# Kernel optimization log

Hardware: AMD Instinct MI355X
Metric: run time of the kernel (lower is better)

## Reference

```python
import jax, jax.numpy as jnp
import numpy as np

EPS = 1e-05  # matches module EPS buffer

def setup_inputs() -> dict:
    key = jax.random.key(0)
    ks = jax.random.split(key, 7)
    B, IN, OUT = 1024, 4096, 4096
    init_log_std = np.log(0.0005).astype(np.float32)
    return {
        "x": jax.random.normal(ks[0], (B, IN), dtype=jnp.float32),
        "weight_mean": jax.random.normal(ks[1], (OUT, IN), dtype=jnp.float32) * (IN ** -0.5),
        "weight_std_param": jnp.full((OUT, IN), init_log_std, dtype=jnp.float32) + 0.01 * jax.random.normal(ks[2], (OUT, IN), dtype=jnp.float32),
        "bias_mean": jax.random.normal(ks[3], (OUT,), dtype=jnp.float32) * (IN ** -0.5),
        "bias_std_param": jnp.full((OUT,), init_log_std, dtype=jnp.float32) + 0.01 * jax.random.normal(ks[4], (OUT,), dtype=jnp.float32),
        "noise_w": jax.random.normal(ks[5], (OUT, IN), dtype=jnp.float32),
        "noise_b": jax.random.normal(ks[6], (OUT,), dtype=jnp.float32),
    }

def reference(x, weight_mean, weight_std_param, bias_mean, bias_std_param, noise_w, noise_b):
    # weight_std = clamp(exp(param), min=EPS); sample = mean + noise * std
    w_std = jnp.maximum(jnp.exp(weight_std_param), EPS)
    b_std = jnp.maximum(jnp.exp(bias_std_param), EPS)
    weight = weight_mean + noise_w * w_std          # [OUT, IN]
    bias = bias_mean + noise_b * b_std              # [OUT]
    # F.linear: x @ weight.T + bias
    return jnp.einsum("bi,oi->bo", x, weight) + bias
```

## Files before the change

### kernel.cpp

```cpp
#include <hip/hip_runtime.h>
#include <stdint.h>

#define EPS 1e-5f

typedef short bf16x8 __attribute__((ext_vector_type(8)));
typedef float f32x4 __attribute__((ext_vector_type(4)));

constexpr int M = 1024, N = 4096, K = 4096;
constexpr int BM = 64, BN = 128, BK = 64;
constexpr int NTK = K / BK;

constexpr int PREP_BLOCKS = 2048;
constexpr int64_t W4 = (int64_t)N * K / 4;
constexpr int64_t X4 = (int64_t)M * K / 4;
constexpr int W4_PER_BLK = (int)(W4 / PREP_BLOCKS);
constexpr int X4_PER_BLK = (int)(X4 / PREP_BLOCKS);
static_assert(W4 % PREP_BLOCKS == 0 && X4 % PREP_BLOCKS == 0, "divide");

__device__ __forceinline__ unsigned short f2bf(float f) {
  union { float f; uint32_t u; } v; v.f = f;
  uint32_t r = (v.u + 0x7fffu + ((v.u >> 16) & 1u)) >> 16;
  return (unsigned short)r;
}

__device__ __forceinline__ void gload16(const void* g, void* l) {
  __builtin_amdgcn_global_load_lds(
      (const __attribute__((address_space(1))) void*)(uintptr_t)g,
      (__attribute__((address_space(3))) void*)(uintptr_t)l, 16, 0, 0);
}

__device__ __forceinline__ void cvt8(const f32x4& a0, const f32x4& a1,
                                     const f32x4& s0, const f32x4& s1,
                                     const f32x4& n0, const f32x4& n1,
                                     bf16x8& o) {
  o[0] = (short)f2bf(a0[0] + n0[0] * fmaxf(__expf(s0[0]), EPS));
  o[1] = (short)f2bf(a0[1] + n0[1] * fmaxf(__expf(s0[1]), EPS));
  o[2] = (short)f2bf(a0[2] + n0[2] * fmaxf(__expf(s0[2]), EPS));
  o[3] = (short)f2bf(a0[3] + n0[3] * fmaxf(__expf(s0[3]), EPS));
  o[4] = (short)f2bf(a1[0] + n1[0] * fmaxf(__expf(s1[0]), EPS));
  o[5] = (short)f2bf(a1[1] + n1[1] * fmaxf(__expf(s1[1]), EPS));
  o[6] = (short)f2bf(a1[2] + n1[2] * fmaxf(__expf(s1[2]), EPS));
  o[7] = (short)f2bf(a1[3] + n1[3] * fmaxf(__expf(s1[3]), EPS));
}

__global__ __launch_bounds__(256) void prep_kernel(
    const float* __restrict__ wm, const float* __restrict__ wsp,
    const float* __restrict__ nw, const float* __restrict__ bm,
    const float* __restrict__ bsp, const float* __restrict__ nb,
    const float* __restrict__ x,
    unsigned short* __restrict__ w_bf, unsigned short* __restrict__ x_bf,
    float* __restrict__ bias)
{
  const int tid = threadIdx.x;
  const int bid = blockIdx.x;
  const f32x4* wm4  = (const f32x4*)wm;
  const f32x4* wsp4 = (const f32x4*)wsp;
  const f32x4* nw4  = (const f32x4*)nw;
  const f32x4* x4   = (const f32x4*)x;
  bf16x8* wb8 = (bf16x8*)w_bf;
  bf16x8* xb8 = (bf16x8*)x_bf;

  {
    const int64_t base4 = (int64_t)bid * W4_PER_BLK;
    const int64_t base8 = base4 >> 1;
#pragma unroll
    for (int it = 0; it < 4; ++it) {
      const int p = it * 256 + tid;
      const int64_t i = base4 + (int64_t)p * 2;
      f32x4 a0 = wm4[i],  a1 = wm4[i + 1];
      f32x4 s0 = wsp4[i], s1 = wsp4[i + 1];
      f32x4 n0 = nw4[i],  n1 = nw4[i + 1];
      bf16x8 o;
      cvt8(a0, a1, s0, s1, n0, n1, o);
      wb8[base8 + p] = o;
    }
  }

  {
    const int64_t base4 = (int64_t)bid * X4_PER_BLK;
    const int64_t i = base4 + (int64_t)tid * 2;
    f32x4 v0 = x4[i], v1 = x4[i + 1];
    bf16x8 o;
    o[0] = (short)f2bf(v0[0]); o[1] = (short)f2bf(v0[1]);
    o[2] = (short)f2bf(v0[2]); o[3] = (short)f2bf(v0[3]);
    o[4] = (short)f2bf(v1[0]); o[5] = (short)f2bf(v1[1]);
    o[6] = (short)f2bf(v1[2]); o[7] = (short)f2bf(v1[3]);
    xb8[(base4 >> 1) + tid] = o;
  }

  const int64_t gt = (int64_t)bid * 256 + tid;
  if (gt < N / 4) {
    float4 a = ((const float4*)bm)[gt];
    float4 s = ((const float4*)bsp)[gt];
    float4 n = ((const float4*)nb)[gt];
    float4 o;
    o.x = a.x + n.x * fmaxf(__expf(s.x), EPS);
    o.y = a.y + n.y * fmaxf(__expf(s.y), EPS);
    o.z = a.z + n.z * fmaxf(__expf(s.z), EPS);
    o.w = a.w + n.w * fmaxf(__expf(s.w), EPS);
    ((float4*)bias)[gt] = o;
  }
}

__global__ __launch_bounds__(256) void gemm_kernel(
    const unsigned short* __restrict__ Abf,
    const unsigned short* __restrict__ Bbf,
    const float* __restrict__ bias,
    float* __restrict__ out)
{
  __shared__ unsigned short lds_mem[2][(BM + BN) * BK];

  const int nwg = gridDim.x;
  const int bid = blockIdx.x;
  const int lid = (bid % 8) * (nwg / 8) + bid / 8;
  const int bc = lid >> 4;
  const int br = lid & 15;

  const int tid = threadIdx.x;
  const int lane = tid & 63;
  const int wid = tid >> 6;

  const int srow = wid * 8 + (lane >> 3);
  const int scol = (((lane & 7) ^ (lane >> 3)) * 8);
  const unsigned short* gA = Abf + (int64_t)(br * BM + srow) * K + scol;
  const unsigned short* gB = Bbf + (int64_t)(bc * BN + srow) * K + scol;

  unsigned short* ldsA0 = &lds_mem[0][0];
  unsigned short* ldsB0 = &lds_mem[0][BM * BK];
  unsigned short* ldsA1 = &lds_mem[1][0];
  unsigned short* ldsB1 = &lds_mem[1][BM * BK];
  const int woff = wid * 8 * BK;

  auto stage = [&](int b, int t) {
    const unsigned short* ga = gA + t * BK;
    const unsigned short* gb = gB + t * BK;
    unsigned short* la = (b ? ldsA1 : ldsA0) + woff;
    unsigned short* lb = (b ? ldsB1 : ldsB0) + woff;
    gload16(ga,          la);
    gload16(ga + 32 * K, la + 32 * BK);
    gload16(gb,          lb);
    gload16(gb + 32 * K, lb + 32 * BK);
    gload16(gb + 64 * K, lb + 64 * BK);
    gload16(gb + 96 * K, lb + 96 * BK);
  };

  f32x4 acc[2][4] = {};
  const int fr = lane & 15;
  const int hi = lane >> 4;
  const int rl = lane & 7;
  const int c0 = ((hi ^ rl) << 3);
  const int c1 = (((4 + hi) ^ rl) << 3);
  const int am = (wid >> 1) * 32;
  const int an = (wid & 1) * 64;

  stage(0, 0);

  int cur = 0;
  for (int t = 0; t < NTK; ++t) {
    __syncthreads();
    if (t + 1 < NTK) stage(cur ^ 1, t + 1);
    const unsigned short* lA = cur ? ldsA1 : ldsA0;
    const unsigned short* lB = cur ? ldsB1 : ldsB0;
#pragma unroll
    for (int kk = 0; kk < 2; ++kk) {
      const int c = kk ? c1 : c0;
      bf16x8 a0 = *(const bf16x8*)&lA[(am +  0 + fr) * BK + c];
      bf16x8 a1 = *(const bf16x8*)&lA[(am + 16 + fr) * BK + c];
      bf16x8 b0 = *(const bf16x8*)&lB[(an +  0 + fr) * BK + c];
      bf16x8 b1 = *(const bf16x8*)&lB[(an + 16 + fr) * BK + c];
      bf16x8 b2 = *(const bf16x8*)&lB[(an + 32 + fr) * BK + c];
      bf16x8 b3 = *(const bf16x8*)&lB[(an + 48 + fr) * BK + c];
      acc[0][0] = __builtin_amdgcn_mfma_f32_16x16x32_bf16(a0, b0, acc[0][0], 0, 0, 0);
      acc[0][1] = __builtin_amdgcn_mfma_f32_16x16x32_bf16(a0, b1, acc[0][1], 0, 0, 0);
      acc[0][2] = __builtin_amdgcn_mfma_f32_16x16x32_bf16(a0, b2, acc[0][2], 0, 0, 0);
      acc[0][3] = __builtin_amdgcn_mfma_f32_16x16x32_bf16(a0, b3, acc[0][3], 0, 0, 0);
      acc[1][0] = __builtin_amdgcn_mfma_f32_16x16x32_bf16(a1, b0, acc[1][0], 0, 0, 0);
      acc[1][1] = __builtin_amdgcn_mfma_f32_16x16x32_bf16(a1, b1, acc[1][1], 0, 0, 0);
      acc[1][2] = __builtin_amdgcn_mfma_f32_16x16x32_bf16(a1, b2, acc[1][2], 0, 0, 0);
      acc[1][3] = __builtin_amdgcn_mfma_f32_16x16x32_bf16(a1, b3, acc[1][3], 0, 0, 0);
    }
    cur ^= 1;
  }

  const int orow0 = br * BM + am + (lane >> 4) * 4;
  const int ocol0 = bc * BN + an + fr;
#pragma unroll
  for (int i = 0; i < 2; ++i) {
#pragma unroll
    for (int j = 0; j < 4; ++j) {
      const int col = ocol0 + j * 16;
      const float bv = bias[col];
      const int row = orow0 + i * 16;
#pragma unroll
      for (int r = 0; r < 4; ++r)
        out[(int64_t)(row + r) * N + col] = acc[i][j][r] + bv;
    }
  }
}

__global__ __launch_bounds__(256) void fallback_kernel(
    const float* __restrict__ x, const float* __restrict__ wm,
    const float* __restrict__ wsp, const float* __restrict__ bm,
    const float* __restrict__ bsp, const float* __restrict__ nw,
    const float* __restrict__ nb, float* __restrict__ out)
{
  int64_t idx = (int64_t)blockIdx.x * 256 + threadIdx.x;
  if (idx >= (int64_t)M * N) return;
  int b = (int)(idx >> 12);
  int o = (int)(idx & (N - 1));
  const float* xr = x + (int64_t)b * K;
  const float* wmr = wm + (int64_t)o * K;
  const float* wsr = wsp + (int64_t)o * K;
  const float* nwr = nw + (int64_t)o * K;
  float s = 0.f;
  for (int k = 0; k < K; ++k)
    s += xr[k] * (wmr[k] + nwr[k] * fmaxf(__expf(wsr[k]), EPS));
  out[idx] = s + bm[o] + nb[o] * fmaxf(__expf(bsp[o]), EPS);
}

extern "C" void kernel_launch(void* const* d_in, const int* in_sizes, int n_in,
                              void* d_out, int out_size, void* d_ws, size_t ws_size,
                              hipStream_t stream) {
  const float* x   = (const float*)d_in[0];
  const float* wm  = (const float*)d_in[1];
  const float* wsp = (const float*)d_in[2];
  const float* bm  = (const float*)d_in[3];
  const float* bsp = (const float*)d_in[4];
  const float* nw  = (const float*)d_in[5];
  const float* nb  = (const float*)d_in[6];
  float* out = (float*)d_out;

  const size_t w_bytes = (size_t)N * K * 2;
  const size_t x_bytes = (size_t)M * K * 2;
  const size_t b_bytes = (size_t)N * 4;
  if (ws_size < w_bytes + x_bytes + b_bytes) {
    fallback_kernel<<<(int)(((int64_t)M * N + 255) / 256), 256, 0, stream>>>(
        x, wm, wsp, bm, bsp, nw, nb, out);
    return;
  }

  char* ws = (char*)d_ws;
  unsigned short* w_bf = (unsigned short*)ws;
  unsigned short* x_bf = (unsigned short*)(ws + w_bytes);
  float* bias = (float*)(ws + w_bytes + x_bytes);

  prep_kernel<<<PREP_BLOCKS, 256, 0, stream>>>(wm, wsp, nw, bm, bsp, nb, x, w_bf, x_bf, bias);
  gemm_kernel<<<(M / BM) * (N / BN), 256, 0, stream>>>(x_bf, w_bf, bias, out);
}
```

Before: 84.03 us.

## Enlarge GEMM tile to 128x128 and add triple-buffered LDS prefetch

Doubles the M tile of the bf16 MFMA GEMM so each wave computes a 64x64 sub-tile, which raises operand reuse per LDS read and halves the number of blocks. It also replaces the double buffer with a three-stage LDS ring, prefetching two K-steps ahead and using explicit vmcnt waits plus raw barriers instead of __syncthreads. The aim is to cut global and LDS traffic per FLOP and hide load latency better. In exchange the grid shrinks to 256 blocks, roughly one per CU, and register and LDS use per block grow, which reduces occupancy and the ability to hide latency by switching waves.

After: 92.78 us. 10.4% more time.

```diff
diff --git a/kernel.cpp b/kernel.cpp
--- a/kernel.cpp
+++ b/kernel.cpp
@@ -7,8 +7,9 @@
 typedef float f32x4 __attribute__((ext_vector_type(4)));
 
 constexpr int M = 1024, N = 4096, K = 4096;
-constexpr int BM = 64, BN = 128, BK = 64;
+constexpr int BM = 128, BN = 128, BK = 64;
 constexpr int NTK = K / BK;
+constexpr int GEMM_GRID = (M / BM) * (N / BN);
 
 constexpr int PREP_BLOCKS = 2048;
 constexpr int64_t W4 = (int64_t)N * K / 4;
@@ -75,7 +76,6 @@
       wb8[base8 + p] = o;
     }
   }
-
   {
     const int64_t base4 = (int64_t)bid * X4_PER_BLK;
     const int64_t i = base4 + (int64_t)tid * 2;
@@ -87,7 +87,6 @@
     o[6] = (short)f2bf(v1[2]); o[7] = (short)f2bf(v1[3]);
     xb8[(base4 >> 1) + tid] = o;
   }
-
   const int64_t gt = (int64_t)bid * 256 + tid;
   if (gt < N / 4) {
     float4 a = ((const float4*)bm)[gt];
@@ -108,84 +107,87 @@
     const float* __restrict__ bias,
     float* __restrict__ out)
 {
-  __shared__ unsigned short lds_mem[2][(BM + BN) * BK];
+  __shared__ unsigned short lds_mem[3][(BM + BN) * BK];
 
   const int nwg = gridDim.x;
   const int bid = blockIdx.x;
   const int lid = (bid % 8) * (nwg / 8) + bid / 8;
-  const int bc = lid >> 4;
-  const int br = lid & 15;
+  const int bc = lid >> 3;
+  const int br = lid & 7;
 
   const int tid = threadIdx.x;
   const int lane = tid & 63;
   const int wid = tid >> 6;
 
   const int srow = wid * 8 + (lane >> 3);
-  const int scol = (((lane & 7) ^ (lane >> 3)) * 8);
+  const int scol = ((lane & 7) ^ (lane >> 3)) * 8;
   const unsigned short* gA = Abf + (int64_t)(br * BM + srow) * K + scol;
   const unsigned short* gB = Bbf + (int64_t)(bc * BN + srow) * K + scol;
-
-  unsigned short* ldsA0 = &lds_mem[0][0];
-  unsigned short* ldsB0 = &lds_mem[0][BM * BK];
-  unsigned short* ldsA1 = &lds_mem[1][0];
-  unsigned short* ldsB1 = &lds_mem[1][BM * BK];
   const int woff = wid * 8 * BK;
 
   auto stage = [&](int b, int t) {
     const unsigned short* ga = gA + t * BK;
     const unsigned short* gb = gB + t * BK;
-    unsigned short* la = (b ? ldsA1 : ldsA0) + woff;
-    unsigned short* lb = (b ? ldsB1 : ldsB0) + woff;
-    gload16(ga,          la);
-    gload16(ga + 32 * K, la + 32 * BK);
-    gload16(gb,          lb);
-    gload16(gb + 32 * K, lb + 32 * BK);
-    gload16(gb + 64 * K, lb + 64 * BK);
-    gload16(gb + 96 * K, lb + 96 * BK);
+    unsigned short* la = &lds_mem[b][0] + woff;
+    unsigned short* lb = &lds_mem[b][BM * BK] + woff;
+#pragma unroll
+    for (int p = 0; p < 4; ++p) {
+      gload16(ga + p * 32 * K, la + p * 32 * BK);
+      gload16(gb + p * 32 * K, lb + p * 32 * BK);
+    }
   };
 
-  f32x4 acc[2][4] = {};
+  f32x4 acc[4][4] = {};
   const int fr = lane & 15;
   const int hi = lane >> 4;
   const int rl = lane & 7;
   const int c0 = ((hi ^ rl) << 3);
   const int c1 = (((4 + hi) ^ rl) << 3);
-  const int am = (wid >> 1) * 32;
+  const int am = (wid >> 1) * 64;
   const int an = (wid & 1) * 64;
 
   stage(0, 0);
+  stage(1, 1);
 
   int cur = 0;
   for (int t = 0; t < NTK; ++t) {
-    __syncthreads();
-    if (t + 1 < NTK) stage(cur ^ 1, t + 1);
-    const unsigned short* lA = cur ? ldsA1 : ldsA0;
-    const unsigned short* lB = cur ? ldsB1 : ldsB0;
+    if (t + 2 < NTK) {
+      int nxt = cur + 2; if (nxt >= 3) nxt -= 3;
+      stage(nxt, t + 2);
+      asm volatile("s_waitcnt vmcnt(16)" ::: "memory");
+    } else if (t + 1 < NTK) {
+      asm volatile("s_waitcnt vmcnt(8)" ::: "memory");
+    } else {
+      asm volatile("s_waitcnt vmcnt(0)" ::: "memory");
+    }
+    __builtin_amdgcn_s_barrier();
+    __builtin_amdgcn_sched_barrier(0);
+    const unsigned short* lA = &lds_mem[cur][0];
+    const unsigned short* lB = &lds_mem[cur][BM * BK];
 #pragma unroll
     for (int kk = 0; kk < 2; ++kk) {
       const int c = kk ? c1 : c0;
-      bf16x8 a0 = *(const bf16x8*)&lA[(am +  0 + fr) * BK + c];
-      bf16x8 a1 = *(const bf16x8*)&lA[(am + 16 + fr) * BK + c];
-      bf16x8 b0 = *(const bf16x8*)&lB[(an +  0 + fr) * BK + c];
-      bf16x8 b1 = *(const bf16x8*)&lB[(an + 16 + fr) * BK + c];
-      bf16x8 b2 = *(const bf16x8*)&lB[(an + 32 + fr) * BK + c];
-      bf16x8 b3 = *(const bf16x8*)&lB[(an + 48 + fr) * BK + c];
-      acc[0][0] = __builtin_amdgcn_mfma_f32_16x16x32_bf16(a0, b0, acc[0][0], 0, 0, 0);
-      acc[0][1] = __builtin_amdgcn_mfma_f32_16x16x32_bf16(a0, b1, acc[0][1], 0, 0, 0);
-      acc[0][2] = __builtin_amdgcn_mfma_f32_16x16x32_bf16(a0, b2, acc[0][2], 0, 0, 0);
-      acc[0][3] = __builtin_amdgcn_mfma_f32_16x16x32_bf16(a0, b3, acc[0][3], 0, 0, 0);
-      acc[1][0] = __builtin_amdgcn_mfma_f32_16x16x32_bf16(a1, b0, acc[1][0], 0, 0, 0);
-      acc[1][1] = __builtin_amdgcn_mfma_f32_16x16x32_bf16(a1, b1, acc[1][1], 0, 0, 0);
-      acc[1][2] = __builtin_amdgcn_mfma_f32_16x16x32_bf16(a1, b2, acc[1][2], 0, 0, 0);
-      acc[1][3] = __builtin_amdgcn_mfma_f32_16x16x32_bf16(a1, b3, acc[1][3], 0, 0, 0);
-    }
-    cur ^= 1;
-  }
-
-  const int orow0 = br * BM + am + (lane >> 4) * 4;
+      bf16x8 a[4], b[4];
+#pragma unroll
+      for (int i = 0; i < 4; ++i) {
+        a[i] = *(const bf16x8*)&lA[(am + 16 * i + fr) * BK + c];
+        b[i] = *(const bf16x8*)&lB[(an + 16 * i + fr) * BK + c];
+      }
+#pragma unroll
+      for (int i = 0; i < 4; ++i)
+#pragma unroll
+        for (int j = 0; j < 4; ++j)
+          acc[i][j] = __builtin_amdgcn_mfma_f32_16x16x32_bf16(a[i], b[j], acc[i][j], 0, 0, 0);
+    }
+    __builtin_amdgcn_sched_barrier(0);
+    __builtin_amdgcn_s_barrier();
+    cur = (cur == 2) ? 0 : cur + 1;
+  }
+
+  const int orow0 = br * BM + am + hi * 4;
   const int ocol0 = bc * BN + an + fr;
 #pragma unroll
-  for (int i = 0; i < 2; ++i) {
+  for (int i = 0; i < 4; ++i) {
 #pragma unroll
     for (int j = 0; j < 4; ++j) {
       const int col = ocol0 + j * 16;
@@ -245,5 +247,5 @@
   float* bias = (float*)(ws + w_bytes + x_bytes);
 
   prep_kernel<<<PREP_BLOCKS, 256, 0, stream>>>(wm, wsp, nw, bm, bsp, nb, x, w_bf, x_bf, bias);
-  gemm_kernel<<<(M / BM) * (N / BN), 256, 0, stream>>>(x_bf, w_bf, bias, out);
-}
+  gemm_kernel<<<GEMM_GRID, 256, 0, stream>>>(x_bf, w_bf, bias, out);
+}
```

## Triple-buffer GEMM LDS stages with explicit vmcnt waits and raw barriers

Applied to the files above, without the earlier changes.

Moves the GEMM main loop from double to triple buffering in LDS, prefetching two K-tiles ahead. Explicit s_waitcnt vmcnt counts wait only for the tile about to be consumed, with raw s_barrier calls before and after compute, replacing __syncthreads. The goal is to keep more global loads in flight and avoid draining all outstanding loads each iteration. In exchange, LDS use per block grows by half, which may lower occupancy, and correctness depends on the hand-set vmcnt counts.

New measurement: 84.99 us. No clear change (+1.1%).

```diff
diff --git a/kernel.cpp b/kernel.cpp
--- a/kernel.cpp
+++ b/kernel.cpp
@@ -9,6 +9,7 @@
 constexpr int M = 1024, N = 4096, K = 4096;
 constexpr int BM = 64, BN = 128, BK = 64;
 constexpr int NTK = K / BK;
+constexpr int GEMM_GRID = (M / BM) * (N / BN);
 
 constexpr int PREP_BLOCKS = 2048;
 constexpr int64_t W4 = (int64_t)N * K / 4;
@@ -75,7 +76,6 @@
       wb8[base8 + p] = o;
     }
   }
-
   {
     const int64_t base4 = (int64_t)bid * X4_PER_BLK;
     const int64_t i = base4 + (int64_t)tid * 2;
@@ -87,7 +87,6 @@
     o[6] = (short)f2bf(v1[2]); o[7] = (short)f2bf(v1[3]);
     xb8[(base4 >> 1) + tid] = o;
   }
-
   const int64_t gt = (int64_t)bid * 256 + tid;
   if (gt < N / 4) {
     float4 a = ((const float4*)bm)[gt];
@@ -108,7 +107,7 @@
     const float* __restrict__ bias,
     float* __restrict__ out)
 {
-  __shared__ unsigned short lds_mem[2][(BM + BN) * BK];
+  __shared__ unsigned short lds_mem[3][(BM + BN) * BK];
 
   const int nwg = gridDim.x;
   const int bid = blockIdx.x;
@@ -121,21 +120,16 @@
   const int wid = tid >> 6;
 
   const int srow = wid * 8 + (lane >> 3);
-  const int scol = (((lane & 7) ^ (lane >> 3)) * 8);
+  const int scol = ((lane & 7) ^ (lane >> 3)) * 8;
   const unsigned short* gA = Abf + (int64_t)(br * BM + srow) * K + scol;
   const unsigned short* gB = Bbf + (int64_t)(bc * BN + srow) * K + scol;
-
-  unsigned short* ldsA0 = &lds_mem[0][0];
-  unsigned short* ldsB0 = &lds_mem[0][BM * BK];
-  unsigned short* ldsA1 = &lds_mem[1][0];
-  unsigned short* ldsB1 = &lds_mem[1][BM * BK];
   const int woff = wid * 8 * BK;
 
   auto stage = [&](int b, int t) {
     const unsigned short* ga = gA + t * BK;
     const unsigned short* gb = gB + t * BK;
-    unsigned short* la = (b ? ldsA1 : ldsA0) + woff;
-    unsigned short* lb = (b ? ldsB1 : ldsB0) + woff;
+    unsigned short* la = &lds_mem[b][0] + woff;
+    unsigned short* lb = &lds_mem[b][BM * BK] + woff;
     gload16(ga,          la);
     gload16(ga + 32 * K, la + 32 * BK);
     gload16(gb,          lb);
@@ -154,13 +148,22 @@
   const int an = (wid & 1) * 64;
 
   stage(0, 0);
+  stage(1, 1);
 
   int cur = 0;
   for (int t = 0; t < NTK; ++t) {
-    __syncthreads();
-    if (t + 1 < NTK) stage(cur ^ 1, t + 1);
-    const unsigned short* lA = cur ? ldsA1 : ldsA0;
-    const unsigned short* lB = cur ? ldsB1 : ldsB0;
+    if (t + 2 < NTK) {
+      int nb = cur + 2; if (nb >= 3) nb -= 3;
+      stage(nb, t + 2);
+      asm volatile("s_waitcnt vmcnt(12)" ::: "memory");
+    } else if (t + 1 < NTK) {
+      asm volatile("s_waitcnt vmcnt(6)" ::: "memory");
+    } else {
+      asm volatile("s_waitcnt vmcnt(0)" ::: "memory");
+    }
+    __builtin_amdgcn_s_barrier();
+    const unsigned short* lA = &lds_mem[cur][0];
+    const unsigned short* lB = &lds_mem[cur][BM * BK];
 #pragma unroll
     for (int kk = 0; kk < 2; ++kk) {
       const int c = kk ? c1 : c0;
@@ -179,10 +182,11 @@
       acc[1][2] = __builtin_amdgcn_mfma_f32_16x16x32_bf16(a1, b2, acc[1][2], 0, 0, 0);
       acc[1][3] = __builtin_amdgcn_mfma_f32_16x16x32_bf16(a1, b3, acc[1][3], 0, 0, 0);
     }
-    cur ^= 1;
-  }
-
-  const int orow0 = br * BM + am + (lane >> 4) * 4;
+    __builtin_amdgcn_s_barrier();
+    cur = (cur == 2) ? 0 : cur + 1;
+  }
+
+  const int orow0 = br * BM + am + hi * 4;
   const int ocol0 = bc * BN + an + fr;
 #pragma unroll
   for (int i = 0; i < 2; ++i) {
@@ -245,5 +249,5 @@
   float* bias = (float*)(ws + w_bytes + x_bytes);
 
   prep_kernel<<<PREP_BLOCKS, 256, 0, stream>>>(wm, wsp, nw, bm, bsp, nb, x, w_bf, x_bf, bias);
-  gemm_kernel<<<(M / BM) * (N / BN), 256, 0, stream>>>(x_bf, w_bf, bias, out);
-}
+  gemm_kernel<<<GEMM_GRID, 256, 0, stream>>>(x_bf, w_bf, bias, out);
+}
```

## Split K in halves to overlap second-half weight prep with first-half GEMM

Applied to the files above, without the earlier changes.

Splits the K dimension into two halves. The first kernel converts the first half of weights and x to bf16 along with the bias. A middle kernel runs producer blocks that convert the second half concurrently with consumer blocks doing the first-half GEMM into the output, and a last kernel does the second-half GEMM, accumulating into the output and adding bias. The aim is to hide the bandwidth-heavy prep under GEMM compute, at the cost of an extra fp32 read and write of the output and a third launch, with producer and consumer blocks contending for bandwidth.

New measurement: 90.65 us. 7.9% more time.

```diff
diff --git a/kernel.cpp b/kernel.cpp
--- a/kernel.cpp
+++ b/kernel.cpp
@@ -8,14 +8,13 @@
 
 constexpr int M = 1024, N = 4096, K = 4096;
 constexpr int BM = 64, BN = 128, BK = 64;
-constexpr int NTK = K / BK;
-
-constexpr int PREP_BLOCKS = 2048;
-constexpr int64_t W4 = (int64_t)N * K / 4;
-constexpr int64_t X4 = (int64_t)M * K / 4;
-constexpr int W4_PER_BLK = (int)(W4 / PREP_BLOCKS);
-constexpr int X4_PER_BLK = (int)(X4 / PREP_BLOCKS);
-static_assert(W4 % PREP_BLOCKS == 0 && X4 % PREP_BLOCKS == 0, "divide");
+constexpr int KH = K / 2;
+constexpr int NTKH = KH / BK;
+constexpr int CONS_BLOCKS = (M / BM) * (N / BN);
+constexpr int PROD_BLOCKS = 256;
+constexpr int K0_BLOCKS = 1024;
+constexpr int64_t WPAIRS_H = (int64_t)N * KH / 8;
+constexpr int64_t XPAIRS_H = (int64_t)M * KH / 8;
 
 __device__ __forceinline__ unsigned short f2bf(float f) {
   union { float f; uint32_t u; } v; v.f = f;
@@ -43,99 +42,85 @@
   o[7] = (short)f2bf(a1[3] + n1[3] * fmaxf(__expf(s1[3]), EPS));
 }
 
-__global__ __launch_bounds__(256) void prep_kernel(
+__device__ __forceinline__ void prep_half(
+    int half, int nb, int bi, int tid,
     const float* __restrict__ wm, const float* __restrict__ wsp,
-    const float* __restrict__ nw, const float* __restrict__ bm,
-    const float* __restrict__ bsp, const float* __restrict__ nb,
-    const float* __restrict__ x,
-    unsigned short* __restrict__ w_bf, unsigned short* __restrict__ x_bf,
-    float* __restrict__ bias)
-{
-  const int tid = threadIdx.x;
-  const int bid = blockIdx.x;
+    const float* __restrict__ nw, const float* __restrict__ x,
+    unsigned short* __restrict__ w_bf, unsigned short* __restrict__ x_bf)
+{
   const f32x4* wm4  = (const f32x4*)wm;
   const f32x4* wsp4 = (const f32x4*)wsp;
   const f32x4* nw4  = (const f32x4*)nw;
   const f32x4* x4   = (const f32x4*)x;
   bf16x8* wb8 = (bf16x8*)w_bf;
   bf16x8* xb8 = (bf16x8*)x_bf;
-
-  {
-    const int64_t base4 = (int64_t)bid * W4_PER_BLK;
-    const int64_t base8 = base4 >> 1;
-#pragma unroll
-    for (int it = 0; it < 4; ++it) {
-      const int p = it * 256 + tid;
-      const int64_t i = base4 + (int64_t)p * 2;
-      f32x4 a0 = wm4[i],  a1 = wm4[i + 1];
-      f32x4 s0 = wsp4[i], s1 = wsp4[i + 1];
-      f32x4 n0 = nw4[i],  n1 = nw4[i + 1];
+  const int hc4 = half * (KH / 4);
+  const int hc8 = half * (KH / 8);
+
+  const int wpb = (int)(WPAIRS_H / nb);
+  const int wmac = wpb / 1024;
+  const int64_t wp0 = (int64_t)bi * wpb;
+  for (int mi = 0; mi < wmac; ++mi) {
+    f32x4 a[4][2], s[4][2], n[4][2];
+    int64_t rr[4]; int pc[4];
+#pragma unroll
+    for (int j = 0; j < 4; ++j) {
+      const int64_t p = wp0 + mi * 1024 + j * 256 + tid;
+      rr[j] = p >> 8; pc[j] = (int)(p & 255);
+      const int64_t i4 = rr[j] * (K / 4) + hc4 + pc[j] * 2;
+      a[j][0] = wm4[i4];  a[j][1] = wm4[i4 + 1];
+      s[j][0] = wsp4[i4]; s[j][1] = wsp4[i4 + 1];
+      n[j][0] = nw4[i4];  n[j][1] = nw4[i4 + 1];
+    }
+#pragma unroll
+    for (int j = 0; j < 4; ++j) {
       bf16x8 o;
-      cvt8(a0, a1, s0, s1, n0, n1, o);
-      wb8[base8 + p] = o;
-    }
-  }
-
-  {
-    const int64_t base4 = (int64_t)bid * X4_PER_BLK;
-    const int64_t i = base4 + (int64_t)tid * 2;
-    f32x4 v0 = x4[i], v1 = x4[i + 1];
+      cvt8(a[j][0], a[j][1], s[j][0], s[j][1], n[j][0], n[j][1], o);
+      wb8[rr[j] * (K / 8) + hc8 + pc[j]] = o;
+    }
+  }
+
+  const int xpb = (int)(XPAIRS_H / nb);
+  const int xit = xpb / 256;
+  const int64_t xp0 = (int64_t)bi * xpb;
+  for (int it = 0; it < xit; ++it) {
+    const int64_t p = xp0 + it * 256 + tid;
+    const int64_t row = p >> 8; const int pc = (int)(p & 255);
+    const int64_t i4 = row * (K / 4) + hc4 + pc * 2;
+    f32x4 v0 = x4[i4], v1 = x4[i4 + 1];
     bf16x8 o;
     o[0] = (short)f2bf(v0[0]); o[1] = (short)f2bf(v0[1]);
     o[2] = (short)f2bf(v0[2]); o[3] = (short)f2bf(v0[3]);
     o[4] = (short)f2bf(v1[0]); o[5] = (short)f2bf(v1[1]);
     o[6] = (short)f2bf(v1[2]); o[7] = (short)f2bf(v1[3]);
-    xb8[(base4 >> 1) + tid] = o;
-  }
-
-  const int64_t gt = (int64_t)bid * 256 + tid;
-  if (gt < N / 4) {
-    float4 a = ((const float4*)bm)[gt];
-    float4 s = ((const float4*)bsp)[gt];
-    float4 n = ((const float4*)nb)[gt];
-    float4 o;
-    o.x = a.x + n.x * fmaxf(__expf(s.x), EPS);
-    o.y = a.y + n.y * fmaxf(__expf(s.y), EPS);
-    o.z = a.z + n.z * fmaxf(__expf(s.z), EPS);
-    o.w = a.w + n.w * fmaxf(__expf(s.w), EPS);
-    ((float4*)bias)[gt] = o;
-  }
-}
-
-__global__ __launch_bounds__(256) void gemm_kernel(
-    const unsigned short* __restrict__ Abf,
-    const unsigned short* __restrict__ Bbf,
-    const float* __restrict__ bias,
-    float* __restrict__ out)
-{
-  __shared__ unsigned short lds_mem[2][(BM + BN) * BK];
-
-  const int nwg = gridDim.x;
-  const int bid = blockIdx.x;
-  const int lid = (bid % 8) * (nwg / 8) + bid / 8;
+    xb8[row * (K / 8) + hc8 + pc] = o;
+  }
+}
+
+__device__ __forceinline__ void gemm_half(
+    int cbid, int kbase, bool accum, int tid,
+    const unsigned short* __restrict__ Abf, const unsigned short* __restrict__ Bbf,
+    const float* __restrict__ biasbuf, float* __restrict__ out,
+    unsigned short* lds0)
+{
+  const int lane = tid & 63;
+  const int wid = tid >> 6;
+
+  const int lid = (cbid % 8) * (CONS_BLOCKS / 8) + cbid / 8;
   const int bc = lid >> 4;
   const int br = lid & 15;
 
-  const int tid = threadIdx.x;
-  const int lane = tid & 63;
-  const int wid = tid >> 6;
-
   const int srow = wid * 8 + (lane >> 3);
-  const int scol = (((lane & 7) ^ (lane >> 3)) * 8);
-  const unsigned short* gA = Abf + (int64_t)(br * BM + srow) * K + scol;
-  const unsigned short* gB = Bbf + (int64_t)(bc * BN + srow) * K + scol;
-
-  unsigned short* ldsA0 = &lds_mem[0][0];
-  unsigned short* ldsB0 = &lds_mem[0][BM * BK];
-  unsigned short* ldsA1 = &lds_mem[1][0];
-  unsigned short* ldsB1 = &lds_mem[1][BM * BK];
+  const int scol = ((lane & 7) ^ (lane >> 3)) * 8;
+  const unsigned short* gA = Abf + (int64_t)(br * BM + srow) * K + kbase + scol;
+  const unsigned short* gB = Bbf + (int64_t)(bc * BN + srow) * K + kbase + scol;
   const int woff = wid * 8 * BK;
 
   auto stage = [&](int b, int t) {
     const unsigned short* ga = gA + t * BK;
     const unsigned short* gb = gB + t * BK;
-    unsigned short* la = (b ? ldsA1 : ldsA0) + woff;
-    unsigned short* lb = (b ? ldsB1 : ldsB0) + woff;
+    unsigned short* la = lds0 + b * ((BM + BN) * BK) + woff;
+    unsigned short* lb = la + BM * BK;
     gload16(ga,          la);
     gload16(ga + 32 * K, la + 32 * BK);
     gload16(gb,          lb);
@@ -156,11 +141,11 @@
   stage(0, 0);
 
   int cur = 0;
-  for (int t = 0; t < NTK; ++t) {
+  for (int t = 0; t < NTKH; ++t) {
     __syncthreads();
-    if (t + 1 < NTK) stage(cur ^ 1, t + 1);
-    const unsigned short* lA = cur ? ldsA1 : ldsA0;
-    const unsigned short* lB = cur ? ldsB1 : ldsB0;
+    if (t + 1 < NTKH) stage(cur ^ 1, t + 1);
+    const unsigned short* lA = lds0 + cur * ((BM + BN) * BK);
+    const unsigned short* lB = lA + BM * BK;
 #pragma unroll
     for (int kk = 0; kk < 2; ++kk) {
       const int c = kk ? c1 : c0;
@@ -182,20 +167,70 @@
     cur ^= 1;
   }
 
-  const int orow0 = br * BM + am + (lane >> 4) * 4;
+  const int orow0 = br * BM + am + hi * 4;
   const int ocol0 = bc * BN + an + fr;
 #pragma unroll
-  for (int i = 0; i < 2; ++i) {
-#pragma unroll
-    for (int j = 0; j < 4; ++j) {
-      const int col = ocol0 + j * 16;
-      const float bv = bias[col];
+  for (int j = 0; j < 4; ++j) {
+    const int col = ocol0 + j * 16;
+    const float bv = accum ? biasbuf[col] : 0.0f;
+#pragma unroll
+    for (int i = 0; i < 2; ++i) {
       const int row = orow0 + i * 16;
 #pragma unroll
-      for (int r = 0; r < 4; ++r)
-        out[(int64_t)(row + r) * N + col] = acc[i][j][r] + bv;
-    }
-  }
+      for (int r = 0; r < 4; ++r) {
+        const int64_t oi = (int64_t)(row + r) * N + col;
+        float v = acc[i][j][r] + bv;
+        if (accum) v += out[oi];
+        out[oi] = v;
+      }
+    }
+  }
+}
+
+__global__ __launch_bounds__(256) void prep0_kernel(
+    const float* __restrict__ wm, const float* __restrict__ wsp,
+    const float* __restrict__ nw, const float* __restrict__ bm,
+    const float* __restrict__ bsp, const float* __restrict__ nb_,
+    const float* __restrict__ x,
+    unsigned short* __restrict__ w_bf, unsigned short* __restrict__ x_bf,
+    float* __restrict__ bias)
+{
+  prep_half(0, K0_BLOCKS, blockIdx.x, threadIdx.x, wm, wsp, nw, x, w_bf, x_bf);
+  const int gt = blockIdx.x * 256 + threadIdx.x;
+  if (gt < N / 4) {
+    float4 a = ((const float4*)bm)[gt];
+    float4 s = ((const float4*)bsp)[gt];
+    float4 n = ((const float4*)nb_)[gt];
+    float4 o;
+    o.x = a.x + n.x * fmaxf(__expf(s.x), EPS);
+    o.y = a.y + n.y * fmaxf(__expf(s.y), EPS);
+    o.z = a.z + n.z * fmaxf(__expf(s.z), EPS);
+    o.w = a.w + n.w * fmaxf(__expf(s.w), EPS);
+    ((float4*)bias)[gt] = o;
+  }
+}
+
+__global__ __launch_bounds__(256) void mid_kernel(
+    const float* __restrict__ wm, const float* __restrict__ wsp,
+    const float* __restrict__ nw, const float* __restrict__ x,
+    unsigned short* __restrict__ w_bf, unsigned short* __restrict__ x_bf,
+    const float* __restrict__ bias, float* __restrict__ out)
+{
+  __shared__ unsigned short lds_mem[2 * (BM + BN) * BK];
+  if (blockIdx.x < PROD_BLOCKS) {
+    prep_half(1, PROD_BLOCKS, blockIdx.x, threadIdx.x, wm, wsp, nw, x, w_bf, x_bf);
+    return;
+  }
+  gemm_half(blockIdx.x - PROD_BLOCKS, 0, false, threadIdx.x,
+            x_bf, w_bf, bias, out, lds_mem);
+}
+
+__global__ __launch_bounds__(256) void last_kernel(
+    const unsigned short* __restrict__ x_bf, const unsigned short* __restrict__ w_bf,
+    const float* __restrict__ bias, float* __restrict__ out)
+{
+  __shared__ unsigned short lds_mem[2 * (BM + BN) * BK];
+  gemm_half(blockIdx.x, KH, true, threadIdx.x, x_bf, w_bf, bias, out, lds_mem);
 }
 
 __global__ __launch_bounds__(256) void fallback_kernel(
@@ -244,6 +279,9 @@
   unsigned short* x_bf = (unsigned short*)(ws + w_bytes);
   float* bias = (float*)(ws + w_bytes + x_bytes);
 
-  prep_kernel<<<PREP_BLOCKS, 256, 0, stream>>>(wm, wsp, nw, bm, bsp, nb, x, w_bf, x_bf, bias);
-  gemm_kernel<<<(M / BM) * (N / BN), 256, 0, stream>>>(x_bf, w_bf, bias, out);
-}
+  prep0_kernel<<<K0_BLOCKS, 256, 0, stream>>>(wm, wsp, nw, bm, bsp, nb, x,
+                                              w_bf, x_bf, bias);
+  mid_kernel<<<PROD_BLOCKS + CONS_BLOCKS, 256, 0, stream>>>(wm, wsp, nw, x,
+                                                            w_bf, x_bf, bias, out);
+  last_kernel<<<CONS_BLOCKS, 256, 0, stream>>>(x_bf, w_bf, bias, out);
+}
```
